# Optimization experiments

Measured on AMD Instinct MI355X. Metric: run time of the kernel, lower is better.

The kernel has to match this reference:

```python
import jax, jax.numpy as jnp
import numpy as np

B, N, H = 4096, 64, 256

def setup_inputs() -> dict:
    key = jax.random.key(0)
    ks = jax.random.split(key, 6)
    scale = 1.0 / np.sqrt(H)
    return {
        "s_t": jax.random.normal(ks[0], (B, H), dtype=jnp.float32),
        "h": jax.random.normal(ks[1], (1, N, H), dtype=jnp.float32) * scale,
        "w": jax.random.normal(ks[2], (1, N, H), dtype=jnp.float32) * scale,
        "U_w": jax.random.normal(ks[3], (H, H), dtype=jnp.float32) * scale,
        "V_w": jax.random.normal(ks[4], (H, H), dtype=jnp.float32) * scale,
        "W_w": jax.random.normal(ks[5], (H, H), dtype=jnp.float32) * scale,
        "prelu_a": jnp.full((1,), 0.25, dtype=jnp.float32),
    }

def _prelu(x, a):
    return jnp.where(x >= 0, x, a * x)

def reference(s_t, h, w, U_w, V_w, W_w, prelu_a):
    # gate: (h + w) @ s_t^T  -> [B, N]
    g = jax.nn.sigmoid(jnp.einsum('onh,bh->bn', h + w, s_t))[..., None]  # [B,N,1]
    # candidate: U(h) + V(w) + W(s_t), broadcast [1,N,H] + [B,1,H] -> [B,N,H]
    cand = _prelu(
        jnp.einsum('onh,kh->onk', h, U_w)
        + jnp.einsum('onh,kh->onk', w, V_w)
        + (s_t @ W_w.T)[:, None, :],
        prelu_a,
    )
    h_new = h + g * cand  # [B,N,H]
    h_new = h_new / jnp.linalg.norm(h_new, axis=2, keepdims=True)
    return h_new
```

## Files before the change

kernel.cpp:

```cpp
#include <hip/hip_runtime.h>
#include <hip/hip_bf16.h>

#define BATCH 4096
#define NMEM  64
#define HDIM  256
#define MROWS 320

typedef __attribute__((ext_vector_type(8))) short short8;
typedef __attribute__((ext_vector_type(4))) float floatx4;

__device__ __forceinline__ float bf2f(unsigned short u) {
    union { unsigned int i; float f; } v; v.i = ((unsigned int)u) << 16; return v.f;
}
__device__ __forceinline__ unsigned short f2bf(float f) {
    union { float f; unsigned int i; } v; v.f = f;
    unsigned int x = v.i;
    return (unsigned short)((x + 0x7FFFu + ((x >> 16) & 1u)) >> 16);
}
__device__ __forceinline__ short8 pack_bf16x8(float4 f0, float4 f1) {
    short8 a;
    a[0] = (short)f2bf(f0.x); a[1] = (short)f2bf(f0.y);
    a[2] = (short)f2bf(f0.z); a[3] = (short)f2bf(f0.w);
    a[4] = (short)f2bf(f1.x); a[5] = (short)f2bf(f1.y);
    a[6] = (short)f2bf(f1.z); a[7] = (short)f2bf(f1.w);
    return a;
}

__global__ __launch_bounds__(256) void prep_kernel(
    const float* __restrict__ h,
    const float* __restrict__ w,
    const float* __restrict__ U_w,
    const float* __restrict__ V_w,
    const float* __restrict__ W_w,
    unsigned short* __restrict__ M,
    unsigned short* __restrict__ A)
{
    const int bid = blockIdx.x;
    const int t   = threadIdx.x;
    if (bid < 16) {
        const int wv   = t >> 6;
        const int lane = t & 63;
        const int m = lane & 15;
        const int q = lane >> 4;
        const int j0 = bid * 16;

        const float* ah = h   + (size_t)(wv * 16 + m) * HDIM;
        const float* aw = w   + (size_t)(wv * 16 + m) * HDIM;
        const float* bu = U_w + (size_t)(j0 + m) * HDIM;
        const float* bv = V_w + (size_t)(j0 + m) * HDIM;

        floatx4 acc = {0.f, 0.f, 0.f, 0.f};
        #pragma unroll
        for (int ks = 0; ks < 16; ++ks) {
            const float* asrc = (ks < 8) ? ah : aw;
            const float* bsrc = (ks < 8) ? bu : bv;
            const int off = (ks & 7) * 32 + q * 8;
            float4 a0 = *(const float4*)(asrc + off);
            float4 a1 = *(const float4*)(asrc + off + 4);
            float4 b0 = *(const float4*)(bsrc + off);
            float4 b1 = *(const float4*)(bsrc + off + 4);
            acc = __builtin_amdgcn_mfma_f32_16x16x32_bf16(
                pack_bf16x8(a0, a1), pack_bf16x8(b0, b1), acc, 0, 0, 0);
        }
        #pragma unroll
        for (int r = 0; r < 4; ++r)
            A[(size_t)(wv * 16 + q * 4 + r) * HDIM + j0 + m] = f2bf(acc[r]);
    } else {
        const int r0 = (bid - 16) * 20;
        for (int rr = 0; rr < 20; ++rr) {
            const int r = r0 + rr;
            float v;
            if (r < 256) v = W_w[(size_t)r * HDIM + t];
            else         v = h[(size_t)(r - 256) * HDIM + t] + w[(size_t)(r - 256) * HDIM + t];
            M[(size_t)r * HDIM + t] = f2bf(v);
        }
    }
}

__global__ __launch_bounds__(256, 4) void fused_kernel(
    const float* __restrict__ s_t,
    const float* __restrict__ h,
    const unsigned short* __restrict__ M,
    const unsigned short* __restrict__ A,
    const float* __restrict__ prelu_a,
    float* __restrict__ out)
{
    __shared__ float C_lds[16][HDIM];
    __shared__ float g_lds[16][16];

    const int b0 = (blockIdx.x >> 2) * 16;
    const int n0 = (blockIdx.x & 3) * 16;
    const int t    = threadIdx.x;
    const int wave = t >> 6;
    const int lane = t & 63;
    const int m = lane & 15;
    const int q = lane >> 4;

    const float* arow = s_t + (size_t)(b0 + m) * HDIM;
    short8 afrag[8];
    #pragma unroll
    for (int ks = 0; ks < 8; ++ks) {
        const int base = ks * 32 + q * 8;
        afrag[ks] = pack_bf16x8(*(const float4*)(arow + base),
                                *(const float4*)(arow + base + 4));
    }
    #pragma unroll
    for (int i = 0; i < 4; ++i) {
        const int j0 = (wave * 4 + i) * 16;
        const short8* brow = (const short8*)(M + (size_t)(j0 + m) * HDIM);
        floatx4 acc = {0.f, 0.f, 0.f, 0.f};
        #pragma unroll
        for (int ks = 0; ks < 8; ++ks)
            acc = __builtin_amdgcn_mfma_f32_16x16x32_bf16(
                afrag[ks], brow[ks * 4 + q], acc, 0, 0, 0);
        #pragma unroll
        for (int r = 0; r < 4; ++r)
            C_lds[q * 4 + r][j0 + m] = acc[r];
    }
    if (wave == 3) {
        const short8* brow = (const short8*)(M + (size_t)(256 + n0 + m) * HDIM);
        floatx4 acc = {0.f, 0.f, 0.f, 0.f};
        #pragma unroll
        for (int ks = 0; ks < 8; ++ks)
            acc = __builtin_amdgcn_mfma_f32_16x16x32_bf16(
                afrag[ks], brow[ks * 4 + q], acc, 0, 0, 0);
        #pragma unroll
        for (int r = 0; r < 4; ++r)
            g_lds[q * 4 + r][m] = 1.f / (1.f + __expf(-acc[r]));
    }
    __syncthreads();

    const float pa = prelu_a[0];
    const int nl = wave * 4 + q;
    const int n  = n0 + nl;
    const float* hrow = h + (size_t)n * HDIM;
    const unsigned short* Arow = A + (size_t)n * HDIM;

    float hv[16], av[16];
    #pragma unroll
    for (int j = 0; j < 4; ++j) {
        const int k = m * 4 + j * 64;
        float4  h4 = *(const float4*)(hrow + k);
        ushort4 a4 = *(const ushort4*)(Arow + k);
        hv[j * 4 + 0] = h4.x; hv[j * 4 + 1] = h4.y;
        hv[j * 4 + 2] = h4.z; hv[j * 4 + 3] = h4.w;
        av[j * 4 + 0] = bf2f(a4.x); av[j * 4 + 1] = bf2f(a4.y);
        av[j * 4 + 2] = bf2f(a4.z); av[j * 4 + 3] = bf2f(a4.w);
    }

    #pragma unroll 2
    for (int b = 0; b < 16; ++b) {
        const float g = g_lds[b][nl];
        float y[16];
        float ss = 0.f;
        #pragma unroll
        for (int j = 0; j < 4; ++j) {
            const int k = m * 4 + j * 64;
            float4 cv = *(const float4*)(&C_lds[b][k]);
            float x0 = av[j * 4 + 0] + cv.x;
            float x1 = av[j * 4 + 1] + cv.y;
            float x2 = av[j * 4 + 2] + cv.z;
            float x3 = av[j * 4 + 3] + cv.w;
            x0 = (x0 >= 0.f) ? x0 : pa * x0;
            x1 = (x1 >= 0.f) ? x1 : pa * x1;
            x2 = (x2 >= 0.f) ? x2 : pa * x2;
            x3 = (x3 >= 0.f) ? x3 : pa * x3;
            float y0 = hv[j * 4 + 0] + g * x0;
            float y1 = hv[j * 4 + 1] + g * x1;
            float y2 = hv[j * 4 + 2] + g * x2;
            float y3 = hv[j * 4 + 3] + g * x3;
            y[j * 4 + 0] = y0; y[j * 4 + 1] = y1;
            y[j * 4 + 2] = y2; y[j * 4 + 3] = y3;
            ss += y0 * y0 + y1 * y1 + y2 * y2 + y3 * y3;
        }
        ss += __shfl_xor(ss, 1);
        ss += __shfl_xor(ss, 2);
        ss += __shfl_xor(ss, 4);
        ss += __shfl_xor(ss, 8);
        const float rn = rsqrtf(ss);

        float* orow = out + ((size_t)(b0 + b) * NMEM + n) * HDIM;
        #pragma unroll
        for (int j = 0; j < 4; ++j) {
            float4 ov;
            ov.x = y[j * 4 + 0] * rn;
            ov.y = y[j * 4 + 1] * rn;
            ov.z = y[j * 4 + 2] * rn;
            ov.w = y[j * 4 + 3] * rn;
            *(float4*)(orow + m * 4 + j * 64) = ov;
        }
    }
}

extern "C" void kernel_launch(void* const* d_in, const int* in_sizes, int n_in,
                              void* d_out, int out_size, void* d_ws, size_t ws_size,
                              hipStream_t stream) {
    const float* s_t     = (const float*)d_in[0];
    const float* h       = (const float*)d_in[1];
    const float* w       = (const float*)d_in[2];
    const float* U_w     = (const float*)d_in[3];
    const float* V_w     = (const float*)d_in[4];
    const float* W_w     = (const float*)d_in[5];
    const float* prelu_a = (const float*)d_in[6];
    float* out = (float*)d_out;

    unsigned short* M = (unsigned short*)d_ws;
    unsigned short* A = (unsigned short*)((char*)d_ws + MROWS * HDIM * 2);

    prep_kernel<<<32, 256, 0, stream>>>(h, w, U_w, V_w, W_w, M, A);
    fused_kernel<<<(BATCH / 16) * 4, 256, 0, stream>>>(s_t, h, M, A, prelu_a, out);
}
```

Measured before the change: 294.6 us.

## Pre-convert s_t to bf16 in prep kernel, reorder loads, use nontemporal output stores

The prep kernel gains 64 extra blocks that convert s_t to bf16 once into workspace, so each fused block loads packed bf16 fragments instead of converting fp32 rows that are re-read by four blocks each. The fused kernel now issues the h/A row loads before the MFMA phase so they overlap with compute. Output stores become nontemporal to avoid polluting cache with the large streaming output. The prep kernel does more work serially before the main kernel, and the bf16 s_t rounding is unchanged from before.

```diff
diff --git a/kernel.cpp b/kernel.cpp
--- a/kernel.cpp
+++ b/kernel.cpp
@@ -27,13 +27,15 @@
 }
 
 __global__ __launch_bounds__(256) void prep_kernel(
+    const float* __restrict__ s_t,
     const float* __restrict__ h,
     const float* __restrict__ w,
     const float* __restrict__ U_w,
     const float* __restrict__ V_w,
     const float* __restrict__ W_w,
     unsigned short* __restrict__ M,
-    unsigned short* __restrict__ A)
+    unsigned short* __restrict__ A,
+    unsigned short* __restrict__ S)
 {
     const int bid = blockIdx.x;
     const int t   = threadIdx.x;
@@ -65,7 +67,7 @@
         #pragma unroll
         for (int r = 0; r < 4; ++r)
             A[(size_t)(wv * 16 + q * 4 + r) * HDIM + j0 + m] = f2bf(acc[r]);
-    } else {
+    } else if (bid < 32) {
         const int r0 = (bid - 16) * 20;
         for (int rr = 0; rr < 20; ++rr) {
             const int r = r0 + rr;
@@ -74,11 +76,17 @@
             else         v = h[(size_t)(r - 256) * HDIM + t] + w[(size_t)(r - 256) * HDIM + t];
             M[(size_t)r * HDIM + t] = f2bf(v);
         }
+    } else {
+        const int r0 = (bid - 32) * 64;
+        for (int rr = 0; rr < 64; ++rr) {
+            const size_t idx = (size_t)(r0 + rr) * HDIM + t;
+            S[idx] = f2bf(s_t[idx]);
+        }
     }
 }
 
 __global__ __launch_bounds__(256, 4) void fused_kernel(
-    const float* __restrict__ s_t,
+    const unsigned short* __restrict__ S,
     const float* __restrict__ h,
     const unsigned short* __restrict__ M,
     const unsigned short* __restrict__ A,
@@ -96,46 +104,10 @@
     const int m = lane & 15;
     const int q = lane >> 4;
 
-    const float* arow = s_t + (size_t)(b0 + m) * HDIM;
-    short8 afrag[8];
-    #pragma unroll
-    for (int ks = 0; ks < 8; ++ks) {
-        const int base = ks * 32 + q * 8;
-        afrag[ks] = pack_bf16x8(*(const float4*)(arow + base),
-                                *(const float4*)(arow + base + 4));
-    }
-    #pragma unroll
-    for (int i = 0; i < 4; ++i) {
-        const int j0 = (wave * 4 + i) * 16;
-        const short8* brow = (const short8*)(M + (size_t)(j0 + m) * HDIM);
-        floatx4 acc = {0.f, 0.f, 0.f, 0.f};
-        #pragma unroll
-        for (int ks = 0; ks < 8; ++ks)
-            acc = __builtin_amdgcn_mfma_f32_16x16x32_bf16(
-                afrag[ks], brow[ks * 4 + q], acc, 0, 0, 0);
-        #pragma unroll
-        for (int r = 0; r < 4; ++r)
-            C_lds[q * 4 + r][j0 + m] = acc[r];
-    }
-    if (wave == 3) {
-        const short8* brow = (const short8*)(M + (size_t)(256 + n0 + m) * HDIM);
-        floatx4 acc = {0.f, 0.f, 0.f, 0.f};
-        #pragma unroll
-        for (int ks = 0; ks < 8; ++ks)
-            acc = __builtin_amdgcn_mfma_f32_16x16x32_bf16(
-                afrag[ks], brow[ks * 4 + q], acc, 0, 0, 0);
-        #pragma unroll
-        for (int r = 0; r < 4; ++r)
-            g_lds[q * 4 + r][m] = 1.f / (1.f + __expf(-acc[r]));
-    }
-    __syncthreads();
-
-    const float pa = prelu_a[0];
     const int nl = wave * 4 + q;
     const int n  = n0 + nl;
     const float* hrow = h + (size_t)n * HDIM;
     const unsigned short* Arow = A + (size_t)n * HDIM;
-
     float hv[16], av[16];
     #pragma unroll
     for (int j = 0; j < 4; ++j) {
@@ -147,6 +119,40 @@
         av[j * 4 + 0] = bf2f(a4.x); av[j * 4 + 1] = bf2f(a4.y);
         av[j * 4 + 2] = bf2f(a4.z); av[j * 4 + 3] = bf2f(a4.w);
     }
+
+    const short8* srow = (const short8*)(S + (size_t)(b0 + m) * HDIM);
+    short8 afrag[8];
+    #pragma unroll
+    for (int ks = 0; ks < 8; ++ks)
+        afrag[ks] = srow[ks * 4 + q];
+
+    #pragma unroll
+    for (int i = 0; i < 4; ++i) {
+        const int j0 = (wave * 4 + i) * 16;
+        const short8* brow = (const short8*)(M + (size_t)(j0 + m) * HDIM);
+        floatx4 acc = {0.f, 0.f, 0.f, 0.f};
+        #pragma unroll
+        for (int ks = 0; ks < 8; ++ks)
+            acc = __builtin_amdgcn_mfma_f32_16x16x32_bf16(
+                afrag[ks], brow[ks * 4 + q], acc, 0, 0, 0);
+        #pragma unroll
+        for (int r = 0; r < 4; ++r)
+            C_lds[q * 4 + r][j0 + m] = acc[r];
+    }
+    if (wave == 3) {
+        const short8* brow = (const short8*)(M + (size_t)(256 + n0 + m) * HDIM);
+        floatx4 acc = {0.f, 0.f, 0.f, 0.f};
+        #pragma unroll
+        for (int ks = 0; ks < 8; ++ks)
+            acc = __builtin_amdgcn_mfma_f32_16x16x32_bf16(
+                afrag[ks], brow[ks * 4 + q], acc, 0, 0, 0);
+        #pragma unroll
+        for (int r = 0; r < 4; ++r)
+            g_lds[q * 4 + r][m] = 1.f / (1.f + __expf(-acc[r]));
+    }
+    __syncthreads();
+
+    const float pa = prelu_a[0];
 
     #pragma unroll 2
     for (int b = 0; b < 16; ++b) {
@@ -182,12 +188,12 @@
         float* orow = out + ((size_t)(b0 + b) * NMEM + n) * HDIM;
         #pragma unroll
         for (int j = 0; j < 4; ++j) {
-            float4 ov;
-            ov.x = y[j * 4 + 0] * rn;
-            ov.y = y[j * 4 + 1] * rn;
-            ov.z = y[j * 4 + 2] * rn;
-            ov.w = y[j * 4 + 3] * rn;
-            *(float4*)(orow + m * 4 + j * 64) = ov;
+            floatx4 ov;
+            ov[0] = y[j * 4 + 0] * rn;
+            ov[1] = y[j * 4 + 1] * rn;
+            ov[2] = y[j * 4 + 2] * rn;
+            ov[3] = y[j * 4 + 3] * rn;
+            __builtin_nontemporal_store(ov, (floatx4*)(orow + m * 4 + j * 64));
         }
     }
 }
@@ -206,7 +212,8 @@
 
     unsigned short* M = (unsigned short*)d_ws;
     unsigned short* A = (unsigned short*)((char*)d_ws + MROWS * HDIM * 2);
-
-    prep_kernel<<<32, 256, 0, stream>>>(h, w, U_w, V_w, W_w, M, A);
-    fused_kernel<<<(BATCH / 16) * 4, 256, 0, stream>>>(s_t, h, M, A, prelu_a, out);
-}
+    unsigned short* S = (unsigned short*)((char*)d_ws + (MROWS + NMEM) * HDIM * 2);
+
+    prep_kernel<<<96, 256, 0, stream>>>(s_t, h, w, U_w, V_w, W_w, M, A, S);
+    fused_kernel<<<(BATCH / 16) * 4, 256, 0, stream>>>(S, h, M, A, prelu_a, out);
+}
```

Result: no change. 300.2 us (+1.9%).
